# Kernel optimization log

Hardware: AMD Instinct MI355X
Metric: run time of the kernel (lower is better)

Reference implementation:

```python
import jax, jax.numpy as jnp
import numpy as np

N_RAYS = 262144
N_BINS = 127  # num_steps - 1 midpoints


def setup_inputs() -> dict:
    key = jax.random.key(0)
    kb, kw = jax.random.split(key)
    # bins are sorted z-midpoints along each ray: strictly increasing via cumsum
    db = jax.random.uniform(kb, (N_RAYS, N_BINS), dtype=jnp.float32) + 0.01
    bins = 0.2 + jnp.cumsum(db, axis=-1) * (3.8 / N_BINS)  # roughly [near, far]
    weights = jax.random.uniform(kw, (N_RAYS, N_BINS - 1), dtype=jnp.float32)
    return {"bins": bins, "weights": weights, "n_samples": 128}


def reference(bins, weights, n_samples):
    # sample_pdf with det=True (inference path: det = not self.training)
    weights = weights + 1e-5                       # [N, M]
    pdf = weights / jnp.sum(weights, -1, keepdims=True)
    cdf = jnp.cumsum(pdf, -1)
    cdf = jnp.concatenate([jnp.zeros_like(cdf[..., :1]), cdf], -1)  # [N, M+1]
    n = n_samples
    u = jnp.linspace(0.5 / n, 1.0 - 0.5 / n, n, dtype=cdf.dtype)
    u = jnp.broadcast_to(u, cdf.shape[:-1] + (n,))  # [N, S]

    # batched binary search: inds = #{cdf <= u} (right=True)
    inds = jax.vmap(lambda c, uu: jnp.searchsorted(c, uu, side="right"))(cdf, u)
    below = jnp.maximum(inds - 1, 0)
    above = jnp.minimum(inds, cdf.shape[-1] - 1)

    cdf_b = jnp.take_along_axis(cdf, below, axis=-1)
    cdf_a = jnp.take_along_axis(cdf, above, axis=-1)
    bins_b = jnp.take_along_axis(bins, below, axis=-1)
    bins_a = jnp.take_along_axis(bins, above, axis=-1)

    denom = cdf_a - cdf_b
    denom = jnp.where(denom < 1e-5, jnp.ones_like(denom), denom)
    t = (u - cdf_b) / denom
    samples = bins_b + t * (bins_a - bins_b)       # [N, S]
    return samples
```

## Files before the change

### kernel.cpp

```cpp
#include <hip/hip_runtime.h>


#define M     126
#define NBINS 127
#define NS    128
#define RPW   3

template<int CTRL, int RM>
__device__ __forceinline__ float dpp_f(float x) {
    return __builtin_bit_cast(float,
        __builtin_amdgcn_update_dpp(0, __builtin_bit_cast(int, x),
                                    CTRL, RM, 0xf, true));
}
template<int CTRL, int RM>
__device__ __forceinline__ int dpp_i(int x) {
    return __builtin_amdgcn_update_dpp(0, x, CTRL, RM, 0xf, true);
}

__device__ __forceinline__ float wave_iscan_add(float x) {
    x += dpp_f<0x111, 0xf>(x);
    x += dpp_f<0x112, 0xf>(x);
    x += dpp_f<0x114, 0xf>(x);
    x += dpp_f<0x118, 0xf>(x);
    x += dpp_f<0x142, 0xa>(x);
    x += dpp_f<0x143, 0xc>(x);
    return x;
}
__device__ __forceinline__ int wave_iscan_max(int x) {
    x = max(x, dpp_i<0x111, 0xf>(x));
    x = max(x, dpp_i<0x112, 0xf>(x));
    x = max(x, dpp_i<0x114, 0xf>(x));
    x = max(x, dpp_i<0x118, 0xf>(x));
    x = max(x, dpp_i<0x142, 0xa>(x));
    x = max(x, dpp_i<0x143, 0xc>(x));
    return x;
}

__global__ __launch_bounds__(256) void sample_pdf_rank10(
    const float* __restrict__ bins,
    const float* __restrict__ weights,
    float* __restrict__ out,
    int n_rays)
{
    __shared__ int    s_idx[4 * RPW][NS];
    __shared__ float4 s_P[4 * RPW][NS / 2];

    const int wave = threadIdx.x >> 6;
    const int lane = threadIdx.x & 63;
    const int base = (blockIdx.x * 4 + wave) * RPW;

    const int  i0   = min(2 * lane, 126);
    const int  i1   = min(2 * lane + 1, 126);
    const int  iw   = min(2 * lane, 124);
    const bool full = (lane < 63);

    #pragma unroll
    for (int r = 0; r < RPW; ++r)
        *reinterpret_cast<int2*>(&s_idx[wave * RPW + r][2 * lane]) = make_int2(0, 0);

    bool  valid[RPW];
    float b_a[RPW], b_b[RPW], w0[RPW], w1[RPW], rw0[RPW], rw1[RPW];
    #pragma unroll
    for (int r = 0; r < RPW; ++r) {
        const int ry = base + r;
        valid[r] = (ry < n_rays);
        const int ryu = __builtin_amdgcn_readfirstlane(valid[r] ? ry : n_rays - 1);
        const float* wrow = weights + (size_t)ryu * M;
        const float* brow = bins    + (size_t)ryu * NBINS;
        b_a[r] = brow[i0];
        b_b[r] = brow[i1];
        const float2 ww = *reinterpret_cast<const float2*>(wrow + iw);
        w0[r] = full ? ww.x + 1e-5f : 0.0f;
        w1[r] = full ? ww.y + 1e-5f : 0.0f;
        rw0[r] = __builtin_amdgcn_rcpf(w0[r]);
        rw1[r] = __builtin_amdgcn_rcpf(w1[r]);
    }
    __builtin_amdgcn_wave_barrier();

    const float u0 = fmaf((float)lane, 0.015625f, 0.00390625f);
    const float u1 = u0 + 0.0078125f;

    #pragma unroll
    for (int r = 0; r < RPW; ++r) {
        const float b_c   = dpp_f<0x130, 0xf>(b_a[r]);
        const float pair  = w0[r] + w1[r];
        const float ps    = wave_iscan_add(pair);
        const float total = __shfl(ps, 63, 64);
        const float inv   = __builtin_amdgcn_rcpf(total);
        const float excl  = ps - pair;
        const float c0 = excl * inv;
        const float c1 = (excl + w0[r]) * inv;
        const float c2 = ps * inv;

        const int g0 = (int)ceilf(fmaf(c0, 128.0f, -0.5f));
        const int g1 = (int)ceilf(fmaf(c1, 128.0f, -0.5f));

        const float dA = c1 - c0;
        const float dB = c2 - c1;
        const float fA = (dA < 1e-5f) ? 1.0f : total * rw0[r];
        const float fB = (dB < 1e-5f) ? 1.0f : total * rw1[r];
        const float slA = (b_b[r] - b_a[r]) * fA;
        const float slB = (b_c    - b_b[r]) * fB;
        const float A0  = fmaf(-c0, slA, b_a[r]);
        const float A1  = fmaf(-c1, slB, b_b[r]);

        const int seg = wave * RPW + r;
        s_P[seg][lane] = make_float4(A0, slA, A1, slB);
        if (g0 < NS) atomicMax(&s_idx[seg][g0], 2 * lane);
        if (g1 < NS) atomicMax(&s_idx[seg][g1], 2 * lane + 1);
    }
    __builtin_amdgcn_wave_barrier();

    #pragma unroll
    for (int r = 0; r < RPW; ++r) {
        const int seg = wave * RPW + r;
        const int2 xi = *reinterpret_cast<const int2*>(&s_idx[seg][2 * lane]);
        const int  m  = wave_iscan_max(max(xi.x, xi.y));
        const int  e  = dpp_i<0x138, 0xf>(m);
        const int  K0 = max(e, xi.x);
        const int  K1 = max(K0, xi.y);

        const float2* P = reinterpret_cast<const float2*>(&s_P[seg][0]);
        const float2 p0 = P[K0];
        const float2 p1 = P[K1];
        float2 res;
        res.x = fmaf(u0, p0.y, p0.x);
        res.y = fmaf(u1, p1.y, p1.x);
        if (valid[r]) {
            const int ro = __builtin_amdgcn_readfirstlane(base + r);
            *reinterpret_cast<float2*>(out + (size_t)ro * NS + 2 * lane) = res;
        }
    }
}

extern "C" void kernel_launch(void* const* d_in, const int* in_sizes, int n_in,
                              void* d_out, int out_size, void* d_ws, size_t ws_size,
                              hipStream_t stream) {
    const float* bins    = (const float*)d_in[0];
    const float* weights = (const float*)d_in[1];
    float* out = (float*)d_out;

    const int n_rays = in_sizes[0] / NBINS;
    const int rays_per_block = 4 * RPW;
    const int blocks = (n_rays + rays_per_block - 1) / rays_per_block;
    sample_pdf_rank10<<<blocks, 256, 0, stream>>>(bins, weights, out, n_rays);
}
```

Measured before the change: 72.42 us.

## Convert to persistent grid-stride kernel with register double-buffered ray loads

Replaces the one-block-per-12-rays launch with a fixed grid of 2048 blocks that stride over the rays. Each wave prefetches the next group's bins and weights into registers while it computes the current group, and clears its shared index buffers after use so they can be reused. The aim is to hide global load latency and cut block launch overhead. In exchange it holds more registers for the prefetched group, which may lower occupancy, and it relies on a fixed grid size that may not fill the device well.

```diff
diff --git a/kernel.cpp b/kernel.cpp
--- a/kernel.cpp
+++ b/kernel.cpp
@@ -5,6 +5,7 @@
 #define NBINS 127
 #define NS    128
 #define RPW   3
+#define NBLK  2048
 
 template<int CTRL, int RM>
 __device__ __forceinline__ float dpp_f(float x) {
@@ -36,53 +37,49 @@
     return x;
 }
 
-__global__ __launch_bounds__(256) void sample_pdf_rank10(
-    const float* __restrict__ bins,
-    const float* __restrict__ weights,
-    float* __restrict__ out,
-    int n_rays)
+struct Grp {
+    float  b_a[RPW], b_b[RPW];
+    float2 ww[RPW];
+    bool   valid[RPW];
+    int    base;
+};
+
+__device__ __forceinline__ void load_grp(const float* __restrict__ bins,
+                                         const float* __restrict__ weights,
+                                         int base, int n_rays,
+                                         int i0, int i1, int iw, Grp& g)
 {
-    __shared__ int    s_idx[4 * RPW][NS];
-    __shared__ float4 s_P[4 * RPW][NS / 2];
-
-    const int wave = threadIdx.x >> 6;
-    const int lane = threadIdx.x & 63;
-    const int base = (blockIdx.x * 4 + wave) * RPW;
-
-    const int  i0   = min(2 * lane, 126);
-    const int  i1   = min(2 * lane + 1, 126);
-    const int  iw   = min(2 * lane, 124);
-    const bool full = (lane < 63);
-
-    #pragma unroll
-    for (int r = 0; r < RPW; ++r)
-        *reinterpret_cast<int2*>(&s_idx[wave * RPW + r][2 * lane]) = make_int2(0, 0);
-
-    bool  valid[RPW];
-    float b_a[RPW], b_b[RPW], w0[RPW], w1[RPW], rw0[RPW], rw1[RPW];
+    g.base = base;
     #pragma unroll
     for (int r = 0; r < RPW; ++r) {
         const int ry = base + r;
-        valid[r] = (ry < n_rays);
-        const int ryu = __builtin_amdgcn_readfirstlane(valid[r] ? ry : n_rays - 1);
+        g.valid[r] = (ry < n_rays);
+        const int ryu = __builtin_amdgcn_readfirstlane(g.valid[r] ? ry : n_rays - 1);
+        const float* brow = bins    + (size_t)ryu * NBINS;
         const float* wrow = weights + (size_t)ryu * M;
-        const float* brow = bins    + (size_t)ryu * NBINS;
-        b_a[r] = brow[i0];
-        b_b[r] = brow[i1];
-        const float2 ww = *reinterpret_cast<const float2*>(wrow + iw);
-        w0[r] = full ? ww.x + 1e-5f : 0.0f;
-        w1[r] = full ? ww.y + 1e-5f : 0.0f;
+        g.b_a[r] = brow[i0];
+        g.b_b[r] = brow[i1];
+        g.ww[r]  = *reinterpret_cast<const float2*>(wrow + iw);
+    }
+}
+
+__device__ __forceinline__ void compute_grp(
+    const Grp& g, bool full, int lane, int segbase,
+    int (*s_idx)[NS], float4 (*s_P)[NS / 2],
+    float* __restrict__ out, float u0, float u1)
+{
+    float w0[RPW], w1[RPW], rw0[RPW], rw1[RPW];
+    #pragma unroll
+    for (int r = 0; r < RPW; ++r) {
+        w0[r] = full ? g.ww[r].x + 1e-5f : 0.0f;
+        w1[r] = full ? g.ww[r].y + 1e-5f : 0.0f;
         rw0[r] = __builtin_amdgcn_rcpf(w0[r]);
         rw1[r] = __builtin_amdgcn_rcpf(w1[r]);
     }
-    __builtin_amdgcn_wave_barrier();
-
-    const float u0 = fmaf((float)lane, 0.015625f, 0.00390625f);
-    const float u1 = u0 + 0.0078125f;
 
     #pragma unroll
     for (int r = 0; r < RPW; ++r) {
-        const float b_c   = dpp_f<0x130, 0xf>(b_a[r]);
+        const float b_c   = dpp_f<0x130, 0xf>(g.b_a[r]);
         const float pair  = w0[r] + w1[r];
         const float ps    = wave_iscan_add(pair);
         const float total = __shfl(ps, 63, 64);
@@ -99,12 +96,12 @@
         const float dB = c2 - c1;
         const float fA = (dA < 1e-5f) ? 1.0f : total * rw0[r];
         const float fB = (dB < 1e-5f) ? 1.0f : total * rw1[r];
-        const float slA = (b_b[r] - b_a[r]) * fA;
-        const float slB = (b_c    - b_b[r]) * fB;
-        const float A0  = fmaf(-c0, slA, b_a[r]);
-        const float A1  = fmaf(-c1, slB, b_b[r]);
+        const float slA = (g.b_b[r] - g.b_a[r]) * fA;
+        const float slB = (b_c      - g.b_b[r]) * fB;
+        const float A0  = fmaf(-c0, slA, g.b_a[r]);
+        const float A1  = fmaf(-c1, slB, g.b_b[r]);
 
-        const int seg = wave * RPW + r;
+        const int seg = segbase + r;
         s_P[seg][lane] = make_float4(A0, slA, A1, slB);
         if (g0 < NS) atomicMax(&s_idx[seg][g0], 2 * lane);
         if (g1 < NS) atomicMax(&s_idx[seg][g1], 2 * lane + 1);
@@ -113,7 +110,7 @@
 
     #pragma unroll
     for (int r = 0; r < RPW; ++r) {
-        const int seg = wave * RPW + r;
+        const int seg = segbase + r;
         const int2 xi = *reinterpret_cast<const int2*>(&s_idx[seg][2 * lane]);
         const int  m  = wave_iscan_max(max(xi.x, xi.y));
         const int  e  = dpp_i<0x138, 0xf>(m);
@@ -126,11 +123,57 @@
         float2 res;
         res.x = fmaf(u0, p0.y, p0.x);
         res.y = fmaf(u1, p1.y, p1.x);
-        if (valid[r]) {
-            const int ro = __builtin_amdgcn_readfirstlane(base + r);
+        if (g.valid[r]) {
+            const int ro = __builtin_amdgcn_readfirstlane(g.base + r);
             *reinterpret_cast<float2*>(out + (size_t)ro * NS + 2 * lane) = res;
         }
     }
+
+    #pragma unroll
+    for (int r = 0; r < RPW; ++r)
+        *reinterpret_cast<int2*>(&s_idx[segbase + r][2 * lane]) = make_int2(0, 0);
+    __builtin_amdgcn_wave_barrier();
+}
+
+__global__ __launch_bounds__(256) void sample_pdf_pipe(
+    const float* __restrict__ bins,
+    const float* __restrict__ weights,
+    float* __restrict__ out,
+    int n_rays)
+{
+    __shared__ int    s_idx[4 * RPW][NS];
+    __shared__ float4 s_P[4 * RPW][NS / 2];
+
+    const int wave = threadIdx.x >> 6;
+    const int lane = threadIdx.x & 63;
+    const int gw   = blockIdx.x * 4 + wave;
+    const int segbase = wave * RPW;
+    const int stride  = NBLK * 4 * RPW;
+
+    const int  i0   = min(2 * lane, 126);
+    const int  i1   = min(2 * lane + 1, 126);
+    const int  iw   = min(2 * lane, 124);
+    const bool full = (lane < 63);
+    const float u0 = fmaf((float)lane, 0.015625f, 0.00390625f);
+    const float u1 = u0 + 0.0078125f;
+
+    #pragma unroll
+    for (int r = 0; r < RPW; ++r)
+        *reinterpret_cast<int2*>(&s_idx[segbase + r][2 * lane]) = make_int2(0, 0);
+    __builtin_amdgcn_wave_barrier();
+
+    int base = gw * RPW;
+    if (base >= n_rays) return;
+
+    Grp cur, nxt;
+    load_grp(bins, weights, base, n_rays, i0, i1, iw, cur);
+
+    for (base += stride; base < n_rays; base += stride) {
+        load_grp(bins, weights, base, n_rays, i0, i1, iw, nxt);
+        compute_grp(cur, full, lane, segbase, s_idx, s_P, out, u0, u1);
+        cur = nxt;
+    }
+    compute_grp(cur, full, lane, segbase, s_idx, s_P, out, u0, u1);
 }
 
 extern "C" void kernel_launch(void* const* d_in, const int* in_sizes, int n_in,
@@ -141,7 +184,5 @@
     float* out = (float*)d_out;
 
     const int n_rays = in_sizes[0] / NBINS;
-    const int rays_per_block = 4 * RPW;
-    const int blocks = (n_rays + rays_per_block - 1) / rays_per_block;
-    sample_pdf_rank10<<<blocks, 256, 0, stream>>>(bins, weights, out, n_rays);
+    sample_pdf_pipe<<<NBLK, 256, 0, stream>>>(bins, weights, out, n_rays);
 }
```

New measurement: 80.59 us. 11.3% more time.

## Gather interpolation coefficients via ds_bpermute instead of LDS table, process four rays per wave

Applied to the files above, without the earlier changes.

Removes the per-ray float4 LDS coefficient table. Each output lane now pulls A/slope values from the owning lane with ds_bpermute and selects even or odd with the low bit. The atomic-scatter and gather phases are merged into one loop per ray. RPW rises from 3 to 4 and launch bounds request 8 blocks per SM, which cuts LDS use and adds memory-level parallelism. The cost is eight bpermutes per ray plus possible register pressure from the occupancy hint.

```diff
diff --git a/kernel.cpp b/kernel.cpp
--- a/kernel.cpp
+++ b/kernel.cpp
@@ -4,7 +4,7 @@
 #define M     126
 #define NBINS 127
 #define NS    128
-#define RPW   3
+#define RPW   4
 
 template<int CTRL, int RM>
 __device__ __forceinline__ float dpp_f(float x) {
@@ -36,14 +36,18 @@
     return x;
 }
 
-__global__ __launch_bounds__(256) void sample_pdf_rank10(
+__device__ __forceinline__ float bperm_f(int addr, float v) {
+    return __builtin_bit_cast(float,
+        __builtin_amdgcn_ds_bpermute(addr, __builtin_bit_cast(int, v)));
+}
+
+__global__ __launch_bounds__(256, 8) void sample_pdf_rank12(
     const float* __restrict__ bins,
     const float* __restrict__ weights,
     float* __restrict__ out,
     int n_rays)
 {
-    __shared__ int    s_idx[4 * RPW][NS];
-    __shared__ float4 s_P[4 * RPW][NS / 2];
+    __shared__ int s_idx[4 * RPW][NS];
 
     const int wave = threadIdx.x >> 6;
     const int lane = threadIdx.x & 63;
@@ -58,22 +62,19 @@
     for (int r = 0; r < RPW; ++r)
         *reinterpret_cast<int2*>(&s_idx[wave * RPW + r][2 * lane]) = make_int2(0, 0);
 
-    bool  valid[RPW];
-    float b_a[RPW], b_b[RPW], w0[RPW], w1[RPW], rw0[RPW], rw1[RPW];
+    bool   valid[RPW];
+    float  b_a[RPW], b_b[RPW];
+    float2 ww[RPW];
     #pragma unroll
     for (int r = 0; r < RPW; ++r) {
         const int ry = base + r;
         valid[r] = (ry < n_rays);
         const int ryu = __builtin_amdgcn_readfirstlane(valid[r] ? ry : n_rays - 1);
+        const float* brow = bins    + (size_t)ryu * NBINS;
         const float* wrow = weights + (size_t)ryu * M;
-        const float* brow = bins    + (size_t)ryu * NBINS;
         b_a[r] = brow[i0];
         b_b[r] = brow[i1];
-        const float2 ww = *reinterpret_cast<const float2*>(wrow + iw);
-        w0[r] = full ? ww.x + 1e-5f : 0.0f;
-        w1[r] = full ? ww.y + 1e-5f : 0.0f;
-        rw0[r] = __builtin_amdgcn_rcpf(w0[r]);
-        rw1[r] = __builtin_amdgcn_rcpf(w1[r]);
+        ww[r]  = *reinterpret_cast<const float2*>(wrow + iw);
     }
     __builtin_amdgcn_wave_barrier();
 
@@ -82,14 +83,19 @@
 
     #pragma unroll
     for (int r = 0; r < RPW; ++r) {
-        const float b_c   = dpp_f<0x130, 0xf>(b_a[r]);
-        const float pair  = w0[r] + w1[r];
+        const float w0  = full ? ww[r].x + 1e-5f : 0.0f;
+        const float w1  = full ? ww[r].y + 1e-5f : 0.0f;
+        const float rw0 = __builtin_amdgcn_rcpf(w0);
+        const float rw1 = __builtin_amdgcn_rcpf(w1);
+        const float b_c = dpp_f<0x130, 0xf>(b_a[r]);
+
+        const float pair  = w0 + w1;
         const float ps    = wave_iscan_add(pair);
         const float total = __shfl(ps, 63, 64);
         const float inv   = __builtin_amdgcn_rcpf(total);
         const float excl  = ps - pair;
         const float c0 = excl * inv;
-        const float c1 = (excl + w0[r]) * inv;
+        const float c1 = (excl + w0) * inv;
         const float c2 = ps * inv;
 
         const int g0 = (int)ceilf(fmaf(c0, 128.0f, -0.5f));
@@ -97,35 +103,37 @@
 
         const float dA = c1 - c0;
         const float dB = c2 - c1;
-        const float fA = (dA < 1e-5f) ? 1.0f : total * rw0[r];
-        const float fB = (dB < 1e-5f) ? 1.0f : total * rw1[r];
+        const float fA = (dA < 1e-5f) ? 1.0f : total * rw0;
+        const float fB = (dB < 1e-5f) ? 1.0f : total * rw1;
         const float slA = (b_b[r] - b_a[r]) * fA;
         const float slB = (b_c    - b_b[r]) * fB;
         const float A0  = fmaf(-c0, slA, b_a[r]);
         const float A1  = fmaf(-c1, slB, b_b[r]);
 
-        const int seg = wave * RPW + r;
-        s_P[seg][lane] = make_float4(A0, slA, A1, slB);
-        if (g0 < NS) atomicMax(&s_idx[seg][g0], 2 * lane);
-        if (g1 < NS) atomicMax(&s_idx[seg][g1], 2 * lane + 1);
-    }
-    __builtin_amdgcn_wave_barrier();
+        int* seg = &s_idx[wave * RPW + r][0];
+        if (g0 < NS) atomicMax(&seg[g0], 2 * lane);
+        if (g1 < NS) atomicMax(&seg[g1], 2 * lane + 1);
 
-    #pragma unroll
-    for (int r = 0; r < RPW; ++r) {
-        const int seg = wave * RPW + r;
-        const int2 xi = *reinterpret_cast<const int2*>(&s_idx[seg][2 * lane]);
-        const int  m  = wave_iscan_max(max(xi.x, xi.y));
-        const int  e  = dpp_i<0x138, 0xf>(m);
+        const int2 xi = *reinterpret_cast<const int2*>(&seg[2 * lane]);
+        const int  Mx = wave_iscan_max(max(xi.x, xi.y));
+        const int  e  = dpp_i<0x138, 0xf>(Mx);
         const int  K0 = max(e, xi.x);
         const int  K1 = max(K0, xi.y);
 
-        const float2* P = reinterpret_cast<const float2*>(&s_P[seg][0]);
-        const float2 p0 = P[K0];
-        const float2 p1 = P[K1];
+        const int ad0 = (K0 >> 1) << 2;
+        const int ad1 = (K1 >> 1) << 2;
+        const float a0e = bperm_f(ad0, A0), a0o = bperm_f(ad0, A1);
+        const float s0e = bperm_f(ad0, slA), s0o = bperm_f(ad0, slB);
+        const float a1e = bperm_f(ad1, A0), a1o = bperm_f(ad1, A1);
+        const float s1e = bperm_f(ad1, slA), s1o = bperm_f(ad1, slB);
+        const float Ag0 = (K0 & 1) ? a0o : a0e;
+        const float Sg0 = (K0 & 1) ? s0o : s0e;
+        const float Ag1 = (K1 & 1) ? a1o : a1e;
+        const float Sg1 = (K1 & 1) ? s1o : s1e;
+
         float2 res;
-        res.x = fmaf(u0, p0.y, p0.x);
-        res.y = fmaf(u1, p1.y, p1.x);
+        res.x = fmaf(u0, Sg0, Ag0);
+        res.y = fmaf(u1, Sg1, Ag1);
         if (valid[r]) {
             const int ro = __builtin_amdgcn_readfirstlane(base + r);
             *reinterpret_cast<float2*>(out + (size_t)ro * NS + 2 * lane) = res;
@@ -143,5 +151,5 @@
     const int n_rays = in_sizes[0] / NBINS;
     const int rays_per_block = 4 * RPW;
     const int blocks = (n_rays + rays_per_block - 1) / rays_per_block;
-    sample_pdf_rank10<<<blocks, 256, 0, stream>>>(bins, weights, out, n_rays);
+    sample_pdf_rank12<<<blocks, 256, 0, stream>>>(bins, weights, out, n_rays);
 }
```

After: 73.81 us. About the same (+1.9%).
